# Optimization experiments

Hardware: AMD Instinct MI355X
Metric: run time of the kernel (lower is better)

Reference implementation:

```python
import math
import jax, jax.numpy as jnp
import numpy as np

B, S, DK, DV = 8, 2048, 512, 512

def setup_inputs() -> dict:
    key = jax.random.key(0)
    kq, kk, kv, km = jax.random.split(key, 4)
    Q = jax.random.normal(kq, (B, S, DK), dtype=jnp.float32)
    K = jax.random.normal(kk, (B, S, DK), dtype=jnp.float32)
    V = jax.random.normal(kv, (B, S, DV), dtype=jnp.float32)
    # key-padding mask, True = masked out; broadcasts over query dim
    mask_out = jax.random.randint(km, (B, 1, S), 0, 2).astype(jnp.bool_)
    return {"Q": Q, "K": K, "V": V, "mask_out": mask_out}

def reference(Q, K, V, mask_out):
    scale = math.sqrt(Q.shape[-1])
    # [B, S, S] scores
    scores = jnp.einsum('bqd,bkd->bqk', Q, K) / scale
    scores = jnp.where(mask_out, -jnp.inf, scores)
    attn = jax.nn.softmax(scores, axis=-1)
    # dropout is identity in eval mode (reference baseline)
    return jnp.einsum('bqk,bkv->bqv', attn, V)
```

## Files before the change

### kernel.cpp

```cpp
#include <hip/hip_runtime.h>
#include <stdint.h>
#include <stddef.h>

#define B_ 8
#define S_ 2048
#define D_ 512
#define QT 64
#define KTL 32
#define NIT (S_ / KTL)

typedef __attribute__((ext_vector_type(8))) short short8;
typedef __attribute__((ext_vector_type(4))) float f32x4;

#define OFF_K0  0
#define OFF_K1  32768
#define OFF_ST  65536
#define OFF_P   73728
#define OFF_A   77824
#define OFF_L   78080
#define OFF_M   78336
#define LDS_BYTES 78592

__device__ __forceinline__ void gl_lds16(const void* g, void* l) {
  __builtin_amdgcn_global_load_lds(
      (const __attribute__((address_space(1))) uint32_t*)g,
      (__attribute__((address_space(3))) uint32_t*)l, 16, 0, 0);
}

__device__ __forceinline__ void bar_lgkm() {
  __asm__ __volatile__("" ::: "memory");
  __builtin_amdgcn_s_waitcnt(0xC07F);
  __builtin_amdgcn_s_barrier();
  __asm__ __volatile__("" ::: "memory");
}
__device__ __forceinline__ void bar_vm0() {
  __asm__ __volatile__("" ::: "memory");
  __builtin_amdgcn_s_waitcnt(0x0070);
  __builtin_amdgcn_s_barrier();
  __asm__ __volatile__("" ::: "memory");
}

__device__ __forceinline__ uint32_t f2bf(float f) {
  union { float f; uint32_t u; } x; x.f = f;
  uint32_t r = x.u + 0x7FFFu + ((x.u >> 16) & 1u);
  return r >> 16;
}

__device__ __forceinline__ bool sniff_fp32(const void* p) {
  const uint32_t* w = (const uint32_t*)p;
  bool ok = true;
  #pragma unroll 1
  for (int i = 0; i < 64; ++i) {
    uint32_t e = (w[i] >> 23) & 0xFFu;
    if (!(e == 0u || (e >= 64u && e <= 192u))) ok = false;
  }
  return ok;
}

__device__ __forceinline__ short8 cvt8(const void* src, bool fp32) {
  short8 d;
  if (fp32) {
    const float* s = (const float*)src;
    f32x4 a = *(const f32x4*)s, c = *(const f32x4*)(s + 4);
    #pragma unroll
    for (int j = 0; j < 4; ++j) { d[j] = (short)f2bf(a[j]); d[4 + j] = (short)f2bf(c[j]); }
  } else {
    d = *(const short8*)src;
  }
  return d;
}

__global__ void prep_kernel(const void* __restrict__ K, const void* __restrict__ V,
                            uint16_t* __restrict__ kbf, uint16_t* __restrict__ vt) {
  __shared__ uint32_t vtile[64 * 32];
  bool fp32 = sniff_fp32(K);
  int kt = blockIdx.x, dt = blockIdx.y, b = blockIdx.z;
  int t  = threadIdx.x;
  {
    size_t off = (size_t)b * S_ * D_ + (size_t)(kt * 64 + (t >> 3)) * D_ + dt * 64 + (t & 7) * 8;
    const void* src = fp32 ? (const void*)((const float*)K + off)
                           : (const void*)((const uint16_t*)K + off);
    *(short8*)(kbf + off) = cvt8(src, fp32);
  }
  {
    int key = t >> 3;
    int c0  = (t & 7) * 4;
    size_t off = (size_t)b * S_ * D_ + (size_t)(kt * 64 + key) * D_ + dt * 64 + (t & 7) * 8;
    const void* src = fp32 ? (const void*)((const float*)V + off)
                           : (const void*)((const uint16_t*)V + off);
    short8 d = cvt8(src, fp32);
    const uint32_t* dw = (const uint32_t*)&d;
    #pragma unroll
    for (int i = 0; i < 4; ++i)
      vtile[key * 32 + ((c0 + i + key) & 31)] = dw[i];
  }
  __syncthreads();
  {
    int dvl = t >> 3;
    int kg  = t & 7;
    short8 o;
    #pragma unroll
    for (int j = 0; j < 8; ++j) {
      int key = kg * 8 + j;
      uint32_t wv = vtile[key * 32 + (((dvl >> 1) + key) & 31)];
      o[j] = (short)((dvl & 1) ? (wv >> 16) : (wv & 0xFFFFu));
    }
    *(short8*)(vt + ((size_t)b * D_ + dt * 64 + dvl) * S_ + kt * 64 + kg * 8) = o;
  }
}

__device__ __forceinline__ void stage_K(char* buf, const uint16_t* kg, int w, int lane, int kt) {
  #pragma unroll
  for (int p = 0; p < 4; ++p) {
    int n = p * 8 + w;
    int g = (lane & ~7) | ((lane ^ n) & 7);
    gl_lds16(kg + ((size_t)(kt * KTL + n)) * D_ + g * 8, buf + n * 1024);
  }
}
__device__ __forceinline__ void stage_K_slow(char* buf, const void* kg, bool fp32,
                                             int w, int lane, int kt) {
  #pragma unroll
  for (int p = 0; p < 4; ++p) {
    int n = p * 8 + w;
    size_t off = ((size_t)(kt * KTL + n)) * D_ + lane * 8;
    const void* src = fp32 ? (const void*)((const float*)kg + off)
                           : (const void*)((const uint16_t*)kg + off);
    short8 d = cvt8(src, fp32);
    int s = (lane & ~7) | ((lane ^ n) & 7);
    *(short8*)(buf + n * 1024 + s * 16) = d;
  }
}
__device__ __forceinline__ void stage_V_slow(char* smem, const void* vg, bool fp32,
                                             int w, int lane, int kt) {
  #pragma unroll
  for (int p = 0; p < 4; ++p) {
    int n = p * 8 + w;
    size_t off = ((size_t)(kt * KTL + n)) * D_ + lane * 8;
    const void* src = fp32 ? (const void*)((const float*)vg + off)
                           : (const void*)((const uint16_t*)vg + off);
    short8 d = cvt8(src, fp32);
    *(short8*)(smem + OFF_K1 + n * 1024 + lane * 16) = d;
  }
}

template<bool FAST>
__global__ __launch_bounds__(512, 2)
void attn_kernel(const void* __restrict__ Q, const void* __restrict__ K,
                 const void* __restrict__ V, const void* __restrict__ mask,
                 const uint16_t* __restrict__ kbf, const uint16_t* __restrict__ vtbf,
                 void* __restrict__ out) {
  extern __shared__ char smem[];
  const int tid  = threadIdx.x;
  const int lane = tid & 63;
  const int w    = tid >> 6;
  const int m15  = lane & 15;
  const int kq   = lane >> 4;

  const bool fp32 = sniff_fp32(Q);

  const int b     = blockIdx.x;
  const int qbase = blockIdx.y * QT;
  const int qt_w  = w >> 1;
  const int kh    = w & 1;

  const uint16_t* kgf  = FAST ? (kbf + (size_t)b * S_ * D_) : nullptr;
  const uint16_t* vtg  = FAST ? (vtbf + (size_t)b * D_ * S_) : nullptr;
  const void* kgs = fp32 ? (const void*)((const float*)K + (size_t)b * S_ * D_)
                         : (const void*)((const uint16_t*)K + (size_t)b * S_ * D_);
  const void* vgs = fp32 ? (const void*)((const float*)V + (size_t)b * S_ * D_)
                         : (const void*)((const uint16_t*)V + (size_t)b * S_ * D_);

  if (tid < 64) {
    const uint32_t* mw = (const uint32_t*)mask;
    const uint8_t*  mb = (const uint8_t*)mask;
    bool is64 = true, any_even = false, is32 = true;
    for (int j = 0; j < 64; ++j) {
      uint32_t lo = mw[2 * j], hi = mw[2 * j + 1];
      if (hi != 0u || lo > 1u) is64 = false;
      if (lo) any_even = true;
    }
    is64 = is64 && any_even;
    for (int j = 0; j < 128; ++j) {
      uint32_t x = mw[j];
      if (x != 0u && x != 1u && x != 0x3F800000u) is32 = false;
    }
    uint32_t bits = 0;
    int base = b * S_ + tid * 32;
    for (int e = 0; e < 32; ++e) {
      uint32_t x = is64 ? mw[2 * (base + e)]
                        : (is32 ? mw[base + e] : (uint32_t)mb[base + e]);
      bits |= (x ? 1u : 0u) << e;
    }
    *(uint32_t*)(smem + OFF_M + tid * 4) = bits;
  }

  short8 aq[16];
  {
    size_t q0 = ((size_t)b * S_ + qbase + qt_w * 16 + m15) * D_ + kq * 8;
    #pragma unroll
    for (int sl = 0; sl < 16; ++sl) {
      size_t off = q0 + sl * 32;
      const void* src = fp32 ? (const void*)((const float*)Q + off)
                             : (const void*)((const uint16_t*)Q + off);
      aq[sl] = cvt8(src, fp32);
    }
  }

  f32x4 acc_o[4][4];
  #pragma unroll
  for (int i = 0; i < 4; ++i)
    #pragma unroll
    for (int j = 0; j < 4; ++j)
      acc_o[i][j] = (f32x4){0.f, 0.f, 0.f, 0.f};

  float m_run = -1e30f, l_run = 0.f;
  const float k1 = 0.06375872f;

  if (FAST) stage_K(smem + OFF_K0, kgf, w, lane, 0);

  for (int kt = 0; kt < NIT; ++kt) {
    char* kbuf = smem + ((kt & 1) && FAST ? OFF_K1 : OFF_K0);
    if (FAST) {
      bar_vm0();
    } else {
      __syncthreads();
      stage_K_slow(smem + OFF_K0, kgs, fp32, w, lane, kt);
      stage_V_slow(smem, vgs, fp32, w, lane, kt);
      __syncthreads();
    }

    short8 vf[4];
    if (FAST) {
      #pragma unroll
      for (int ct = 0; ct < 4; ++ct)
        vf[ct] = *(const short8*)(vtg + (size_t)(w * 64 + ct * 16 + m15) * S_
                                  + kt * KTL + kq * 8);
      if (kt < NIT - 1)
        stage_K(smem + ((kt & 1) ? OFF_K0 : OFF_K1), kgf, w, lane, kt + 1);
    }

    int keyg = kt * KTL + kh * 16 + m15;
    float bv = ((*(const uint32_t*)(smem + OFF_M + (keyg >> 5) * 4) >> (keyg & 31)) & 1u)
               ? -3.0e38f : 0.f;

    f32x4 acc_s = (f32x4){0.f, 0.f, 0.f, 0.f};
    #pragma unroll
    for (int sl = 0; sl < 16; ++sl) {
      int n  = kh * 16 + m15;
      int c  = sl * 4 + kq;
      int cs = (c & ~7) | ((c ^ n) & 7);
      short8 bf = *(const short8*)(kbuf + n * 1024 + cs * 16);
      acc_s = __builtin_amdgcn_mfma_f32_16x16x32_bf16(aq[sl], bf, acc_s, 0, 0, 0);
    }

    {
      int key  = kh * 16 + m15;
      int blk  = qt_w * 4 + kq;
      int xblk = blk ^ (key & 15) ^ ((key >> 2) & 3);
      f32x4 sv;
      #pragma unroll
      for (int r = 0; r < 4; ++r) sv[r] = acc_s[r] * k1 + bv;
      *(f32x4*)(smem + OFF_ST + key * 256 + xblk * 16) = sv;
    }
    bar_lgkm();

    {
      int r  = w * 8 + (lane >> 3);
      int k0 = (lane & 7) * 4;
      float u[4];
      #pragma unroll
      for (int i = 0; i < 4; ++i) {
        int k    = k0 + i;
        int xblk = (r >> 2) ^ (k & 15) ^ ((k >> 2) & 3);
        u[i] = *(const float*)(smem + OFF_ST + k * 256 + xblk * 16 + (r & 3) * 4);
      }
      float mt = fmaxf(fmaxf(u[0], u[1]), fmaxf(u[2], u[3]));
      mt = fmaxf(mt, __shfl_xor(mt, 1, 64));
      mt = fmaxf(mt, __shfl_xor(mt, 2, 64));
      mt = fmaxf(mt, __shfl_xor(mt, 4, 64));
      float m_new = fmaxf(m_run, mt);
      float alpha = exp2f(m_run - m_new);
      float s = 0.f;
      #pragma unroll
      for (int i = 0; i < 4; ++i) { u[i] = exp2f(u[i] - m_new); s += u[i]; }
      s += __shfl_xor(s, 1, 64);
      s += __shfl_xor(s, 2, 64);
      s += __shfl_xor(s, 4, 64);
      l_run = l_run * alpha + s;
      m_run = m_new;
      uint2 d;
      d.x = f2bf(u[0]) | (f2bf(u[1]) << 16);
      d.y = f2bf(u[2]) | (f2bf(u[3]) << 16);
      *(uint2*)(smem + OFF_P + r * 64 + k0 * 2) = d;
      if ((lane & 7) == 0) {
        *(float*)(smem + OFF_A + r * 4) = alpha;
        *(float*)(smem + OFF_L + r * 4) = l_run;
      }
    }
    bar_lgkm();

    #pragma unroll
    for (int rt = 0; rt < 4; ++rt) {
      f32x4 al = *(const f32x4*)(smem + OFF_A + (rt * 16 + kq * 4) * 4);
      #pragma unroll
      for (int ct = 0; ct < 4; ++ct) acc_o[rt][ct] *= al;
    }
    short8 ap[4];
    #pragma unroll
    for (int rt = 0; rt < 4; ++rt)
      ap[rt] = *(const short8*)(smem + OFF_P + (rt * 16 + m15) * 64 + kq * 16);
    #pragma unroll
    for (int ct = 0; ct < 4; ++ct) {
      short8 bvv;
      if (FAST) {
        bvv = vf[ct];
      } else {
        #pragma unroll
        for (int j = 0; j < 8; ++j)
          bvv[j] = *(const short*)(smem + OFF_K1 + (kq * 8 + j) * 1024
                                   + (w * 64 + ct * 16 + m15) * 2);
      }
      #pragma unroll
      for (int rt = 0; rt < 4; ++rt)
        acc_o[rt][ct] = __builtin_amdgcn_mfma_f32_16x16x32_bf16(
            ap[rt], bvv, acc_o[rt][ct], 0, 0, 0);
    }
  }

  #pragma unroll
  for (int rt = 0; rt < 4; ++rt) {
    f32x4 lv = *(const f32x4*)(smem + OFF_L + (rt * 16 + kq * 4) * 4);
    f32x4 inv;
    #pragma unroll
    for (int r = 0; r < 4; ++r) inv[r] = lv[r] > 0.f ? 1.f / lv[r] : 0.f;
    #pragma unroll
    for (int ct = 0; ct < 4; ++ct) {
      int col = w * 64 + ct * 16 + m15;
      #pragma unroll
      for (int r = 0; r < 4; ++r) {
        int row = qbase + rt * 16 + kq * 4 + r;
        size_t idx = ((size_t)b * S_ + row) * D_ + col;
        float val = acc_o[rt][ct][r] * inv[r];
        if (fp32) ((float*)out)[idx] = val;
        else      ((uint16_t*)out)[idx] = (uint16_t)f2bf(val);
      }
    }
  }
}

extern "C" void kernel_launch(void* const* d_in, const int* in_sizes, int n_in,
                              void* d_out, int out_size, void* d_ws, size_t ws_size,
                              hipStream_t stream) {
  (void)in_sizes; (void)n_in; (void)out_size;
  const void* Q    = d_in[0];
  const void* K    = d_in[1];
  const void* V    = d_in[2];
  const void* mask = d_in[3];

  const size_t half = (size_t)B_ * S_ * D_ * 2;
  bool fast = ws_size >= 2 * half;

  if (fast) {
    uint16_t* kbf  = (uint16_t*)d_ws;
    uint16_t* vtbf = (uint16_t*)((char*)d_ws + half);
    prep_kernel<<<dim3(32, 8, 8), 512, 0, stream>>>(K, V, kbf, vtbf);
    hipFuncSetAttribute((const void*)attn_kernel<true>,
                        hipFuncAttributeMaxDynamicSharedMemorySize, LDS_BYTES);
    attn_kernel<true><<<dim3(8, S_ / QT), 512, LDS_BYTES, stream>>>(
        Q, K, V, mask, kbf, vtbf, d_out);
  } else {
    hipFuncSetAttribute((const void*)attn_kernel<false>,
                        hipFuncAttributeMaxDynamicSharedMemorySize, LDS_BYTES);
    attn_kernel<false><<<dim3(8, S_ / QT), 512, LDS_BYTES, stream>>>(
        Q, K, V, mask, nullptr, nullptr, d_out);
  }
}
```

Measured before the change: 293.6 us.

## Double key tile to 64 with two score MFMAs per wave and swizzled P

```diff
diff --git a/kernel.cpp b/kernel.cpp
--- a/kernel.cpp
+++ b/kernel.cpp
@@ -6,20 +6,20 @@
 #define S_ 2048
 #define D_ 512
 #define QT 64
-#define KTL 32
+#define KTL 64
 #define NIT (S_ / KTL)
 
 typedef __attribute__((ext_vector_type(8))) short short8;
 typedef __attribute__((ext_vector_type(4))) float f32x4;
 
 #define OFF_K0  0
-#define OFF_K1  32768
-#define OFF_ST  65536
-#define OFF_P   73728
-#define OFF_A   77824
-#define OFF_L   78080
-#define OFF_M   78336
-#define LDS_BYTES 78592
+#define OFF_K1  65536
+#define OFF_ST  131072
+#define OFF_P   147456
+#define OFF_A   155648
+#define OFF_L   155904
+#define OFF_M   156160
+#define LDS_BYTES 156416
 
 __device__ __forceinline__ void gl_lds16(const void* g, void* l) {
   __builtin_amdgcn_global_load_lds(
@@ -111,7 +111,7 @@
 
 __device__ __forceinline__ void stage_K(char* buf, const uint16_t* kg, int w, int lane, int kt) {
   #pragma unroll
-  for (int p = 0; p < 4; ++p) {
+  for (int p = 0; p < 8; ++p) {
     int n = p * 8 + w;
     int g = (lane & ~7) | ((lane ^ n) & 7);
     gl_lds16(kg + ((size_t)(kt * KTL + n)) * D_ + g * 8, buf + n * 1024);
@@ -120,7 +120,7 @@
 __device__ __forceinline__ void stage_K_slow(char* buf, const void* kg, bool fp32,
                                              int w, int lane, int kt) {
   #pragma unroll
-  for (int p = 0; p < 4; ++p) {
+  for (int p = 0; p < 8; ++p) {
     int n = p * 8 + w;
     size_t off = ((size_t)(kt * KTL + n)) * D_ + lane * 8;
     const void* src = fp32 ? (const void*)((const float*)kg + off)
@@ -133,7 +133,7 @@
 __device__ __forceinline__ void stage_V_slow(char* smem, const void* vg, bool fp32,
                                              int w, int lane, int kt) {
   #pragma unroll
-  for (int p = 0; p < 4; ++p) {
+  for (int p = 0; p < 8; ++p) {
     int n = p * 8 + w;
     size_t off = ((size_t)(kt * KTL + n)) * D_ + lane * 8;
     const void* src = fp32 ? (const void*)((const float*)vg + off)
@@ -160,8 +160,8 @@
 
   const int b     = blockIdx.x;
   const int qbase = blockIdx.y * QT;
-  const int qt_w  = w >> 1;
-  const int kh    = w & 1;
+  const int qt    = w >> 1;
+  const int kk0   = (w & 1) * 2;
 
   const uint16_t* kgf  = FAST ? (kbf + (size_t)b * S_ * D_) : nullptr;
   const uint16_t* vtg  = FAST ? (vtbf + (size_t)b * D_ * S_) : nullptr;
@@ -196,7 +196,7 @@
 
   short8 aq[16];
   {
-    size_t q0 = ((size_t)b * S_ + qbase + qt_w * 16 + m15) * D_ + kq * 8;
+    size_t q0 = ((size_t)b * S_ + qbase + qt * 16 + m15) * D_ + kq * 8;
     #pragma unroll
     for (int sl = 0; sl < 16; ++sl) {
       size_t off = q0 + sl * 32;
@@ -229,52 +229,61 @@
       __syncthreads();
     }
 
-    short8 vf[4];
+    short8 vf[4][2];
     if (FAST) {
       #pragma unroll
       for (int ct = 0; ct < 4; ++ct)
-        vf[ct] = *(const short8*)(vtg + (size_t)(w * 64 + ct * 16 + m15) * S_
-                                  + kt * KTL + kq * 8);
+        #pragma unroll
+        for (int kc = 0; kc < 2; ++kc)
+          vf[ct][kc] = *(const short8*)(vtg + (size_t)(w * 64 + ct * 16 + m15) * S_
+                                        + kt * KTL + kc * 32 + kq * 8);
       if (kt < NIT - 1)
         stage_K(smem + ((kt & 1) ? OFF_K0 : OFF_K1), kgf, w, lane, kt + 1);
     }
 
-    int keyg = kt * KTL + kh * 16 + m15;
-    float bv = ((*(const uint32_t*)(smem + OFF_M + (keyg >> 5) * 4) >> (keyg & 31)) & 1u)
-               ? -3.0e38f : 0.f;
-
-    f32x4 acc_s = (f32x4){0.f, 0.f, 0.f, 0.f};
+    const int n0 = kk0 * 16 + m15;
+    const int n1 = n0 + 16;
+    f32x4 acc_s0 = (f32x4){0.f, 0.f, 0.f, 0.f};
+    f32x4 acc_s1 = (f32x4){0.f, 0.f, 0.f, 0.f};
     #pragma unroll
     for (int sl = 0; sl < 16; ++sl) {
-      int n  = kh * 16 + m15;
-      int c  = sl * 4 + kq;
-      int cs = (c & ~7) | ((c ^ n) & 7);
-      short8 bf = *(const short8*)(kbuf + n * 1024 + cs * 16);
-      acc_s = __builtin_amdgcn_mfma_f32_16x16x32_bf16(aq[sl], bf, acc_s, 0, 0, 0);
-    }
-
-    {
-      int key  = kh * 16 + m15;
-      int blk  = qt_w * 4 + kq;
-      int xblk = blk ^ (key & 15) ^ ((key >> 2) & 3);
+      int c   = sl * 4 + kq;
+      int cs0 = (c & ~7) | ((c ^ n0) & 7);
+      int cs1 = (c & ~7) | ((c ^ n1) & 7);
+      short8 b0 = *(const short8*)(kbuf + n0 * 1024 + cs0 * 16);
+      short8 b1 = *(const short8*)(kbuf + n1 * 1024 + cs1 * 16);
+      acc_s0 = __builtin_amdgcn_mfma_f32_16x16x32_bf16(aq[sl], b0, acc_s0, 0, 0, 0);
+      acc_s1 = __builtin_amdgcn_mfma_f32_16x16x32_bf16(aq[sl], b1, acc_s1, 0, 0, 0);
+    }
+
+    #pragma unroll
+    for (int sli = 0; sli < 2; ++sli) {
+      int key  = (sli == 0) ? n0 : n1;
+      int keyg = kt * KTL + key;
+      float bv = ((*(const uint32_t*)(smem + OFF_M + (keyg >> 5) * 4) >> (keyg & 31)) & 1u)
+                 ? -3.0e38f : 0.f;
+      int blk  = qt * 4 + kq;
+      int xblk = blk ^ (key & 15) ^ ((key >> 2) & 3) ^ (((key >> 4) & 3) << 1);
       f32x4 sv;
-      #pragma unroll
-      for (int r = 0; r < 4; ++r) sv[r] = acc_s[r] * k1 + bv;
+      f32x4 as = (sli == 0) ? acc_s0 : acc_s1;
+      #pragma unroll
+      for (int r = 0; r < 4; ++r) sv[r] = as[r] * k1 + bv;
       *(f32x4*)(smem + OFF_ST + key * 256 + xblk * 16) = sv;
     }
     bar_lgkm();
 
     {
       int r  = w * 8 + (lane >> 3);
-      int k0 = (lane & 7) * 4;
-      float u[4];
-      #pragma unroll
-      for (int i = 0; i < 4; ++i) {
+      int k0 = (lane & 7) * 8;
+      float u[8];
+      #pragma unroll
+      for (int i = 0; i < 8; ++i) {
         int k    = k0 + i;
-        int xblk = (r >> 2) ^ (k & 15) ^ ((k >> 2) & 3);
+        int xblk = (r >> 2) ^ (k & 15) ^ ((k >> 2) & 3) ^ (((k >> 4) & 3) << 1);
         u[i] = *(const float*)(smem + OFF_ST + k * 256 + xblk * 16 + (r & 3) * 4);
       }
-      float mt = fmaxf(fmaxf(u[0], u[1]), fmaxf(u[2], u[3]));
+      float mt = fmaxf(fmaxf(fmaxf(u[0], u[1]), fmaxf(u[2], u[3])),
+                       fmaxf(fmaxf(u[4], u[5]), fmaxf(u[6], u[7])));
       mt = fmaxf(mt, __shfl_xor(mt, 1, 64));
       mt = fmaxf(mt, __shfl_xor(mt, 2, 64));
       mt = fmaxf(mt, __shfl_xor(mt, 4, 64));
@@ -282,16 +291,19 @@
       float alpha = exp2f(m_run - m_new);
       float s = 0.f;
       #pragma unroll
-      for (int i = 0; i < 4; ++i) { u[i] = exp2f(u[i] - m_new); s += u[i]; }
+      for (int i = 0; i < 8; ++i) { u[i] = exp2f(u[i] - m_new); s += u[i]; }
       s += __shfl_xor(s, 1, 64);
       s += __shfl_xor(s, 2, 64);
       s += __shfl_xor(s, 4, 64);
       l_run = l_run * alpha + s;
       m_run = m_new;
-      uint2 d;
+      uint4 d;
       d.x = f2bf(u[0]) | (f2bf(u[1]) << 16);
       d.y = f2bf(u[2]) | (f2bf(u[3]) << 16);
-      *(uint2*)(smem + OFF_P + r * 64 + k0 * 2) = d;
+      d.z = f2bf(u[4]) | (f2bf(u[5]) << 16);
+      d.w = f2bf(u[6]) | (f2bf(u[7]) << 16);
+      int g = (lane & 7) ^ (r & 7);
+      *(uint4*)(smem + OFF_P + r * 128 + g * 16) = d;
       if ((lane & 7) == 0) {
         *(float*)(smem + OFF_A + r * 4) = alpha;
         *(float*)(smem + OFF_L + r * 4) = l_run;
@@ -305,25 +317,33 @@
       #pragma unroll
       for (int ct = 0; ct < 4; ++ct) acc_o[rt][ct] *= al;
     }
-    short8 ap[4];
+    short8 ap[4][2];
     #pragma unroll
     for (int rt = 0; rt < 4; ++rt)
-      ap[rt] = *(const short8*)(smem + OFF_P + (rt * 16 + m15) * 64 + kq * 16);
+      #pragma unroll
+      for (int kc = 0; kc < 2; ++kc) {
+        int rr = rt * 16 + m15;
+        int g  = (kc * 4 + kq) ^ (rr & 7);
+        ap[rt][kc] = *(const short8*)(smem + OFF_P + rr * 128 + g * 16);
+      }
     #pragma unroll
     for (int ct = 0; ct < 4; ++ct) {
-      short8 bvv;
-      if (FAST) {
-        bvv = vf[ct];
-      } else {
+      #pragma unroll
+      for (int kc = 0; kc < 2; ++kc) {
+        short8 bvv;
+        if (FAST) {
+          bvv = vf[ct][kc];
+        } else {
+          #pragma unroll
+          for (int j = 0; j < 8; ++j)
+            bvv[j] = *(const short*)(smem + OFF_K1 + (kc * 32 + kq * 8 + j) * 1024
+                                     + (w * 64 + ct * 16 + m15) * 2);
+        }
         #pragma unroll
-        for (int j = 0; j < 8; ++j)
-          bvv[j] = *(const short*)(smem + OFF_K1 + (kq * 8 + j) * 1024
-                                   + (w * 64 + ct * 16 + m15) * 2);
-      }
-      #pragma unroll
-      for (int rt = 0; rt < 4; ++rt)
-        acc_o[rt][ct] = __builtin_amdgcn_mfma_f32_16x16x32_bf16(
-            ap[rt], bvv, acc_o[rt][ct], 0, 0, 0);
+        for (int rt = 0; rt < 4; ++rt)
+          acc_o[rt][ct] = __builtin_amdgcn_mfma_f32_16x16x32_bf16(
+              ap[rt][kc], bvv, acc_o[rt][ct], 0, 0, 0);
+      }
     }
   }
 
```

New measurement: 280.2 us. 4.6% less time.
